# Kernel optimization log

Measured on AMD Instinct MI355X. Metric: run time of the kernel, lower is better.

Reference implementation:

```python
import jax, jax.numpy as jnp
import numpy as np

TEMP = 0.5      # init temperature
EPS = 1e-8      # torch CosineSimilarity eps
B = 4096
D = 512


def setup_inputs() -> dict:
    key = jax.random.key(0)
    k1, k2 = jax.random.split(key)
    return {
        "zis": jax.random.normal(k1, (B, D), dtype=jnp.float32),
        "zjs": jax.random.normal(k2, (B, D), dtype=jnp.float32),
    }


def reference(zis, zjs):
    # representations = cat([zjs, zis]) -> [2B, D]
    reps = jnp.concatenate([zjs, zis], axis=0)
    b = zis.shape[0]
    n = 2 * b

    # cosine similarity matrix [2B, 2B]
    norms = jnp.maximum(jnp.linalg.norm(reps, axis=-1, keepdims=True), EPS)
    z = reps / norms
    sim = jnp.matmul(z, z.T) / TEMP

    # positive for row i is sim[i, (i+B) % 2B]; self-similarity is excluded.
    # CE with label 0 over [pos, negatives] == logsumexp over row (minus diag)
    # minus the positive logit, because pos is exactly the masked pair entry.
    idx = jnp.arange(n)
    pair = (idx + b) % n
    pos = sim[idx, pair]
    sim_masked = jnp.where(jnp.eye(n, dtype=bool), -1e9, sim)  # drop diagonal
    per_row = jax.nn.logsumexp(sim_masked, axis=-1) - pos
    # criterion sums, then divides by 2B -> mean
    return jnp.mean(per_row)
```

## Files before the change

kernel.cpp:

```cpp
#include <hip/hip_runtime.h>

#define N_TOT 8192
#define BHALF 4096
#define D_DIM 512
#define BM 128
#define BK 64
#define NTILE 64
#define NBLOCKS 2080

typedef float f32x4 __attribute__((ext_vector_type(4)));
typedef short s16x8 __attribute__((ext_vector_type(8)));

__device__ __forceinline__ unsigned short f2bf(float x) {
    union { float f; unsigned int u; } v; v.f = x;
    unsigned int lsb = (v.u >> 16) & 1u;
    unsigned int r = v.u + 0x7fffu + lsb;
    return (unsigned short)(r >> 16);
}

__global__ __launch_bounds__(256) void normalize_kernel(
    const float* __restrict__ zis, const float* __restrict__ zjs,
    unsigned short* __restrict__ zb, float* __restrict__ rowsum)
{
    if (blockIdx.x < 32) rowsum[blockIdx.x * 256 + threadIdx.x] = 0.0f;
    int wave = threadIdx.x >> 6;
    int lane = threadIdx.x & 63;
    int row  = blockIdx.x * 4 + wave;
    const float* src = (row < BHALF) ? (zjs + (size_t)row * D_DIM)
                                     : (zis + (size_t)(row - BHALF) * D_DIM);
    const float4* src4 = (const float4*)src;
    float4 v0 = src4[lane * 2];
    float4 v1 = src4[lane * 2 + 1];
    float ss = v0.x*v0.x + v0.y*v0.y + v0.z*v0.z + v0.w*v0.w
             + v1.x*v1.x + v1.y*v1.y + v1.z*v1.z + v1.w*v1.w;
    #pragma unroll
    for (int off = 1; off < 64; off <<= 1) ss += __shfl_xor(ss, off);
    float scale = 1.0f / fmaxf(sqrtf(ss), 1e-8f);

    float vals[8] = {v0.x, v0.y, v0.z, v0.w, v1.x, v1.y, v1.z, v1.w};
    unsigned short u[8];
    #pragma unroll
    for (int i = 0; i < 8; ++i) u[i] = f2bf(vals[i] * scale);
    uint4 o;
    o.x = u[0] | ((unsigned)u[1] << 16);
    o.y = u[2] | ((unsigned)u[3] << 16);
    o.z = u[4] | ((unsigned)u[5] << 16);
    o.w = u[6] | ((unsigned)u[7] << 16);
    ((uint4*)(zb + (size_t)row * D_DIM))[lane] = o;
}

__global__ __launch_bounds__(256) void ntxent_tri_kernel(
    const unsigned short* __restrict__ zb, float* __restrict__ rowsum,
    float* __restrict__ pos_ws)
{
    __shared__ unsigned short As[BM * BK];
    __shared__ unsigned short Bs[BM * BK];
    __shared__ float rsum_lds[BM];
    __shared__ float csum_lds[BM];

    const int tid  = threadIdx.x;
    const int wave = tid >> 6;
    const int lane = tid & 63;
    const int cq   = lane & 15;
    const int quad = lane >> 4;
    const int wr   = wave >> 1;
    const int wc   = wave & 1;

    int g = 0, rem = blockIdx.x;
    while (rem >= 64 * g + 36) { rem -= 64 * g + 36; ++g; }
    int I, J;
    if (rem < 64 * g) { I = rem >> 3; J = 8 * g + (rem & 7); }
    else {
        rem -= 64 * g;
        int ii = 0;
        while (rem >= 8 - ii) { rem -= 8 - ii; ++ii; }
        I = 8 * g + ii;
        J = I + rem;
    }
    const int rowbase = I * BM;
    const int colbase = J * BM;
    const bool diagblk = (I == J);
    const bool posblk  = (J == I + NTILE / 2);

    if (tid < BM) { rsum_lds[tid] = 0.0f; csum_lds[tid] = 0.0f; }

    const int r0  = tid >> 3;
    const int c8s = (tid & 7) ^ (r0 & 7);
    const unsigned short* gA[4];
    const unsigned short* gB[4];
    #pragma unroll
    for (int rnd = 0; rnd < 4; ++rnd) {
        int r = rnd * 32 + r0;
        gA[rnd] = zb + (size_t)(rowbase + r) * D_DIM + c8s * 8;
        gB[rnd] = zb + (size_t)(colbase + r) * D_DIM + c8s * 8;
    }

    int aOff[4], aSw[4], bOff[4], bSw[4];
    #pragma unroll
    for (int t = 0; t < 4; ++t) {
        int ra = wr * 64 + t * 16 + cq;
        int rb = wc * 64 + t * 16 + cq;
        aOff[t] = ra * 64; aSw[t] = ra & 7;
        bOff[t] = rb * 64; bSw[t] = rb & 7;
    }

    f32x4 acc[4][4];
    #pragma unroll
    for (int a = 0; a < 4; ++a)
        #pragma unroll
        for (int b = 0; b < 4; ++b)
            acc[a][b] = (f32x4){0.f, 0.f, 0.f, 0.f};

    for (int kc = 0; kc < D_DIM / BK; ++kc) {
        __syncthreads();
        #pragma unroll
        for (int rnd = 0; rnd < 4; ++rnd) {
            __builtin_amdgcn_global_load_lds(
                (const __attribute__((address_space(1))) unsigned int*)gA[rnd],
                (__attribute__((address_space(3))) unsigned int*)&As[(rnd * 256 + tid) * 8],
                16, 0, 0);
            __builtin_amdgcn_global_load_lds(
                (const __attribute__((address_space(1))) unsigned int*)gB[rnd],
                (__attribute__((address_space(3))) unsigned int*)&Bs[(rnd * 256 + tid) * 8],
                16, 0, 0);
            gA[rnd] += BK; gB[rnd] += BK;
        }
        __syncthreads();

        #pragma unroll
        for (int kk = 0; kk < 2; ++kk) {
            s16x8 af[4], bf[4];
            const int c8a = kk * 4 + quad;
            #pragma unroll
            for (int t = 0; t < 4; ++t) {
                af[t] = *(const s16x8*)&As[aOff[t] + ((c8a ^ aSw[t]) << 3)];
                bf[t] = *(const s16x8*)&Bs[bOff[t] + ((c8a ^ bSw[t]) << 3)];
            }
            #pragma unroll
            for (int ar = 0; ar < 4; ++ar)
                #pragma unroll
                for (int bc = 0; bc < 4; ++bc)
                    acc[ar][bc] = __builtin_amdgcn_mfma_f32_16x16x32_bf16(
                        af[ar], bf[bc], acc[ar][bc], 0, 0, 0);
        }
    }

    if (posblk && wc == wr) {
        #pragma unroll
        for (int ar = 0; ar < 4; ++ar)
            #pragma unroll
            for (int reg = 0; reg < 4; ++reg)
                if (cq == quad * 4 + reg) {
                    int gr = rowbase + wr * 64 + ar * 16 + quad * 4 + reg;
                    pos_ws[gr] = acc[ar][ar][reg] * 2.0f;
                }
    }

    #pragma unroll
    for (int ar = 0; ar < 4; ++ar)
        #pragma unroll
        for (int bc = 0; bc < 4; ++bc)
            #pragma unroll
            for (int reg = 0; reg < 4; ++reg)
                acc[ar][bc][reg] = __expf(acc[ar][bc][reg] * 2.0f);
    if (diagblk && wr == wc) {
        #pragma unroll
        for (int ar = 0; ar < 4; ++ar)
            #pragma unroll
            for (int reg = 0; reg < 4; ++reg)
                if (cq == quad * 4 + reg) acc[ar][ar][reg] = 0.0f;
    }

    #pragma unroll
    for (int ar = 0; ar < 4; ++ar) {
        float rs[4];
        #pragma unroll
        for (int reg = 0; reg < 4; ++reg) {
            float v = acc[ar][0][reg] + acc[ar][1][reg] + acc[ar][2][reg] + acc[ar][3][reg];
            v += __shfl_xor(v, 1); v += __shfl_xor(v, 2);
            v += __shfl_xor(v, 4); v += __shfl_xor(v, 8);
            rs[reg] = v;
        }
        if (cq == 0) {
            #pragma unroll
            for (int reg = 0; reg < 4; ++reg)
                atomicAdd(&rsum_lds[wr * 64 + ar * 16 + quad * 4 + reg], rs[reg]);
        }
    }

    if (!diagblk) {
        #pragma unroll
        for (int bc = 0; bc < 4; ++bc) {
            float cs = 0.0f;
            #pragma unroll
            for (int ar = 0; ar < 4; ++ar)
                #pragma unroll
                for (int reg = 0; reg < 4; ++reg)
                    cs += acc[ar][bc][reg];
            cs += __shfl_xor(cs, 16); cs += __shfl_xor(cs, 32);
            if (quad == 0) atomicAdd(&csum_lds[wc * 64 + bc * 16 + cq], cs);
        }
    }

    __syncthreads();
    if (tid < BM) atomicAdd(&rowsum[rowbase + tid], rsum_lds[tid]);
    else if (!diagblk) atomicAdd(&rowsum[colbase + tid - BM], csum_lds[tid - BM]);
}

__global__ __launch_bounds__(256) void finalize_kernel(
    const float* __restrict__ rowsum, const float* __restrict__ pos_ws,
    float* __restrict__ out)
{
    __shared__ float red[4];
    float s = 0.0f;
    for (int r = threadIdx.x; r < N_TOT; r += 256)
        s += __logf(rowsum[r]) - pos_ws[r & (BHALF - 1)];
    #pragma unroll
    for (int off = 1; off < 64; off <<= 1) s += __shfl_xor(s, off);
    int wave = threadIdx.x >> 6, lane = threadIdx.x & 63;
    if (lane == 0) red[wave] = s;
    __syncthreads();
    if (threadIdx.x == 0)
        out[0] = (red[0] + red[1] + red[2] + red[3]) * (1.0f / N_TOT);
}

extern "C" void kernel_launch(void* const* d_in, const int* in_sizes, int n_in,
                              void* d_out, int out_size, void* d_ws, size_t ws_size,
                              hipStream_t stream) {
    const float* zis = (const float*)d_in[0];
    const float* zjs = (const float*)d_in[1];
    float* rowsum = (float*)d_ws;
    float* pos_ws = (float*)d_ws + N_TOT;
    unsigned short* zb = (unsigned short*)((float*)d_ws + N_TOT + BHALF);
    float* out = (float*)d_out;

    normalize_kernel<<<N_TOT / 4, 256, 0, stream>>>(zis, zjs, zb, rowsum);
    ntxent_tri_kernel<<<NBLOCKS, 256, 0, stream>>>(zb, rowsum, pos_ws);
    finalize_kernel<<<1, 256, 0, stream>>>(rowsum, pos_ws, out);
}
```

Measured before the change: 132.3 us.

## Fuse finalize into GEMM via last-block counter, fold scale into exp2

Folds the 1/T and log2(e) factors into the normalization scale (sqrt(2/ln2)) so the epilogue can use a raw exp2 instead of multiply plus expf, and rescales the positive logit by ln2. The finalize kernel is removed: a done counter lets the last block finishing the triangular GEMM compute the log-sum reduction, saving one launch. LDS for the row and column sums now reuses the A tile buffer, and launch bounds request 5 waves per SIMD. This adds extra barriers, a global atomic counter and fences, and the pre-scaled bf16 inputs change rounding slightly.

New measurement: 182.1 us. 1.38x slower.

```diff
diff --git a/kernel.cpp b/kernel.cpp
--- a/kernel.cpp
+++ b/kernel.cpp
@@ -8,6 +8,9 @@
 #define NTILE 64
 #define NBLOCKS 2080
 
+#define ZSCALE 1.69864368f
+#define LN2F   0.69314718f
+
 typedef float f32x4 __attribute__((ext_vector_type(4)));
 typedef short s16x8 __attribute__((ext_vector_type(8)));
 
@@ -18,11 +21,21 @@
     return (unsigned short)(r >> 16);
 }
 
+__device__ __forceinline__ float fast_exp2(float x) {
+#if __has_builtin(__builtin_amdgcn_exp2f)
+    return __builtin_amdgcn_exp2f(x);
+#else
+    return exp2f(x);
+#endif
+}
+
 __global__ __launch_bounds__(256) void normalize_kernel(
     const float* __restrict__ zis, const float* __restrict__ zjs,
-    unsigned short* __restrict__ zb, float* __restrict__ rowsum)
+    unsigned short* __restrict__ zb, float* __restrict__ rowsum,
+    unsigned int* __restrict__ done_ctr)
 {
     if (blockIdx.x < 32) rowsum[blockIdx.x * 256 + threadIdx.x] = 0.0f;
+    if (blockIdx.x == 32 && threadIdx.x == 0) *done_ctr = 0u;
     int wave = threadIdx.x >> 6;
     int lane = threadIdx.x & 63;
     int row  = blockIdx.x * 4 + wave;
@@ -35,7 +48,7 @@
              + v1.x*v1.x + v1.y*v1.y + v1.z*v1.z + v1.w*v1.w;
     #pragma unroll
     for (int off = 1; off < 64; off <<= 1) ss += __shfl_xor(ss, off);
-    float scale = 1.0f / fmaxf(sqrtf(ss), 1e-8f);
+    float scale = ZSCALE / fmaxf(sqrtf(ss), 1e-8f);
 
     float vals[8] = {v0.x, v0.y, v0.z, v0.w, v1.x, v1.y, v1.z, v1.w};
     unsigned short u[8];
@@ -49,14 +62,13 @@
     ((uint4*)(zb + (size_t)row * D_DIM))[lane] = o;
 }
 
-__global__ __launch_bounds__(256) void ntxent_tri_kernel(
+__global__ __launch_bounds__(256, 5) void ntxent_tri_kernel(
     const unsigned short* __restrict__ zb, float* __restrict__ rowsum,
-    float* __restrict__ pos_ws)
+    float* __restrict__ pos_ws, float* __restrict__ out,
+    unsigned int* __restrict__ done_ctr)
 {
     __shared__ unsigned short As[BM * BK];
     __shared__ unsigned short Bs[BM * BK];
-    __shared__ float rsum_lds[BM];
-    __shared__ float csum_lds[BM];
 
     const int tid  = threadIdx.x;
     const int wave = tid >> 6;
@@ -82,8 +94,6 @@
     const bool diagblk = (I == J);
     const bool posblk  = (J == I + NTILE / 2);
 
-    if (tid < BM) { rsum_lds[tid] = 0.0f; csum_lds[tid] = 0.0f; }
-
     const int r0  = tid >> 3;
     const int c8s = (tid & 7) ^ (r0 & 7);
     const unsigned short* gA[4];
@@ -152,7 +162,8 @@
             for (int reg = 0; reg < 4; ++reg)
                 if (cq == quad * 4 + reg) {
                     int gr = rowbase + wr * 64 + ar * 16 + quad * 4 + reg;
-                    pos_ws[gr] = acc[ar][ar][reg] * 2.0f;
+                    __hip_atomic_store(&pos_ws[gr], acc[ar][ar][reg] * LN2F,
+                                       __ATOMIC_RELAXED, __HIP_MEMORY_SCOPE_AGENT);
                 }
     }
 
@@ -162,7 +173,7 @@
         for (int bc = 0; bc < 4; ++bc)
             #pragma unroll
             for (int reg = 0; reg < 4; ++reg)
-                acc[ar][bc][reg] = __expf(acc[ar][bc][reg] * 2.0f);
+                acc[ar][bc][reg] = fast_exp2(acc[ar][bc][reg]);
     if (diagblk && wr == wc) {
         #pragma unroll
         for (int ar = 0; ar < 4; ++ar)
@@ -170,6 +181,12 @@
             for (int reg = 0; reg < 4; ++reg)
                 if (cq == quad * 4 + reg) acc[ar][ar][reg] = 0.0f;
     }
+
+    float* rsum_lds = (float*)As;
+    float* csum_lds = rsum_lds + BM;
+    __syncthreads();
+    ((float*)As)[tid] = 0.0f;
+    __syncthreads();
 
     #pragma unroll
     for (int ar = 0; ar < 4; ++ar) {
@@ -205,23 +222,32 @@
     __syncthreads();
     if (tid < BM) atomicAdd(&rowsum[rowbase + tid], rsum_lds[tid]);
     else if (!diagblk) atomicAdd(&rowsum[colbase + tid - BM], csum_lds[tid - BM]);
-}
-
-__global__ __launch_bounds__(256) void finalize_kernel(
-    const float* __restrict__ rowsum, const float* __restrict__ pos_ws,
-    float* __restrict__ out)
-{
-    __shared__ float red[4];
-    float s = 0.0f;
-    for (int r = threadIdx.x; r < N_TOT; r += 256)
-        s += __logf(rowsum[r]) - pos_ws[r & (BHALF - 1)];
-    #pragma unroll
-    for (int off = 1; off < 64; off <<= 1) s += __shfl_xor(s, off);
-    int wave = threadIdx.x >> 6, lane = threadIdx.x & 63;
-    if (lane == 0) red[wave] = s;
-    __syncthreads();
-    if (threadIdx.x == 0)
-        out[0] = (red[0] + red[1] + red[2] + red[3]) * (1.0f / N_TOT);
+
+    __shared__ int lastflag;
+    __syncthreads();
+    if (tid == 0) {
+        __threadfence();
+        lastflag = (atomicAdd(done_ctr, 1u) == (unsigned)(NBLOCKS - 1));
+    }
+    __syncthreads();
+    if (lastflag) {
+        __threadfence();
+        float s = 0.0f;
+        for (int r = tid; r < N_TOT; r += 256) {
+            float rsv = __hip_atomic_load(&rowsum[r],
+                                          __ATOMIC_RELAXED, __HIP_MEMORY_SCOPE_AGENT);
+            float pv  = __hip_atomic_load(&pos_ws[r & (BHALF - 1)],
+                                          __ATOMIC_RELAXED, __HIP_MEMORY_SCOPE_AGENT);
+            s += __logf(rsv) - pv;
+        }
+        #pragma unroll
+        for (int off = 1; off < 64; off <<= 1) s += __shfl_xor(s, off);
+        float* red = (float*)Bs;
+        if ((tid & 63) == 0) red[tid >> 6] = s;
+        __syncthreads();
+        if (tid == 0)
+            out[0] = (red[0] + red[1] + red[2] + red[3]) * (1.0f / N_TOT);
+    }
 }
 
 extern "C" void kernel_launch(void* const* d_in, const int* in_sizes, int n_in,
@@ -230,11 +256,11 @@
     const float* zis = (const float*)d_in[0];
     const float* zjs = (const float*)d_in[1];
     float* rowsum = (float*)d_ws;
-    float* pos_ws = (float*)d_ws + N_TOT;
-    unsigned short* zb = (unsigned short*)((float*)d_ws + N_TOT + BHALF);
+    float* pos_ws = rowsum + N_TOT;
+    unsigned int* done_ctr = (unsigned int*)(pos_ws + BHALF);
+    unsigned short* zb = (unsigned short*)(pos_ws + BHALF + 4);
     float* out = (float*)d_out;
 
-    normalize_kernel<<<N_TOT / 4, 256, 0, stream>>>(zis, zjs, zb, rowsum);
-    ntxent_tri_kernel<<<NBLOCKS, 256, 0, stream>>>(zb, rowsum, pos_ws);
-    finalize_kernel<<<1, 256, 0, stream>>>(rowsum, pos_ws, out);
-}
+    normalize_kernel<<<N_TOT / 4, 256, 0, stream>>>(zis, zjs, zb, rowsum, done_ctr);
+    ntxent_tri_kernel<<<NBLOCKS, 256, 0, stream>>>(zb, rowsum, pos_ws, out, done_ctr);
+}
```

## Double-buffer K loop with smaller chunks and fold temperature into normalization for exp2

Applied to the files above, without the earlier changes.

The GEMM main loop now uses two LDS buffers of 32-wide K chunks and issues the next chunk's global-to-LDS loads before computing the current one, gated by a partial vmcnt wait. This is meant to overlap memory latency with MFMA work instead of fully synchronising every chunk. The normalized vectors are pre-scaled by sqrt(2/ln2), so the dot product is already in log2 units and the epilogue uses a raw exp2 instead of a multiply plus exp. The positive logit is rescaled by ln2. The reduction scratch now reuses the A buffer to save LDS. Scaling before bf16 rounding slightly changes numerics.

After: 123.7 us. -6.5%, faster.

```diff
diff --git a/kernel.cpp b/kernel.cpp
--- a/kernel.cpp
+++ b/kernel.cpp
@@ -4,9 +4,14 @@
 #define BHALF 4096
 #define D_DIM 512
 #define BM 128
-#define BK 64
 #define NTILE 64
 #define NBLOCKS 2080
+#define BK2 32
+#define NCHUNK 16
+#define BUFSZ (BM * BK2)
+
+#define ZSCALE 1.69864368f
+#define LN2F   0.69314718f
 
 typedef float f32x4 __attribute__((ext_vector_type(4)));
 typedef short s16x8 __attribute__((ext_vector_type(8)));
@@ -16,6 +21,14 @@
     unsigned int lsb = (v.u >> 16) & 1u;
     unsigned int r = v.u + 0x7fffu + lsb;
     return (unsigned short)(r >> 16);
+}
+
+__device__ __forceinline__ float fast_exp2(float x) {
+#if __has_builtin(__builtin_amdgcn_exp2f)
+    return __builtin_amdgcn_exp2f(x);
+#else
+    return exp2f(x);
+#endif
 }
 
 __global__ __launch_bounds__(256) void normalize_kernel(
@@ -35,7 +48,7 @@
              + v1.x*v1.x + v1.y*v1.y + v1.z*v1.z + v1.w*v1.w;
     #pragma unroll
     for (int off = 1; off < 64; off <<= 1) ss += __shfl_xor(ss, off);
-    float scale = 1.0f / fmaxf(sqrtf(ss), 1e-8f);
+    float scale = ZSCALE / fmaxf(sqrtf(ss), 1e-8f);
 
     float vals[8] = {v0.x, v0.y, v0.z, v0.w, v1.x, v1.y, v1.z, v1.w};
     unsigned short u[8];
@@ -53,10 +66,8 @@
     const unsigned short* __restrict__ zb, float* __restrict__ rowsum,
     float* __restrict__ pos_ws)
 {
-    __shared__ unsigned short As[BM * BK];
-    __shared__ unsigned short Bs[BM * BK];
-    __shared__ float rsum_lds[BM];
-    __shared__ float csum_lds[BM];
+    __shared__ unsigned short As[2 * BUFSZ];
+    __shared__ unsigned short Bs[2 * BUFSZ];
 
     const int tid  = threadIdx.x;
     const int wave = tid >> 6;
@@ -82,26 +93,20 @@
     const bool diagblk = (I == J);
     const bool posblk  = (J == I + NTILE / 2);
 
-    if (tid < BM) { rsum_lds[tid] = 0.0f; csum_lds[tid] = 0.0f; }
-
-    const int r0  = tid >> 3;
-    const int c8s = (tid & 7) ^ (r0 & 7);
-    const unsigned short* gA[4];
-    const unsigned short* gB[4];
-    #pragma unroll
-    for (int rnd = 0; rnd < 4; ++rnd) {
-        int r = rnd * 32 + r0;
-        gA[rnd] = zb + (size_t)(rowbase + r) * D_DIM + c8s * 8;
-        gB[rnd] = zb + (size_t)(colbase + r) * D_DIM + c8s * 8;
-    }
-
-    int aOff[4], aSw[4], bOff[4], bSw[4];
+    const int c8s = (tid & 3) ^ ((tid >> 3) & 3);
+    const unsigned short* pA0 = zb + (size_t)(rowbase + (tid >> 2)) * D_DIM + c8s * 8;
+    const unsigned short* pA1 = pA0 + (size_t)64 * D_DIM;
+    const unsigned short* pB0 = zb + (size_t)(colbase + (tid >> 2)) * D_DIM + c8s * 8;
+    const unsigned short* pB1 = pB0 + (size_t)64 * D_DIM;
+    const int dst0 = tid * 8;
+    const int dst1 = (256 + tid) * 8;
+
+    const int swz = (quad ^ ((cq >> 1) & 3)) << 3;
+    int aOff[4], bOff[4];
     #pragma unroll
     for (int t = 0; t < 4; ++t) {
-        int ra = wr * 64 + t * 16 + cq;
-        int rb = wc * 64 + t * 16 + cq;
-        aOff[t] = ra * 64; aSw[t] = ra & 7;
-        bOff[t] = rb * 64; bSw[t] = rb & 7;
+        aOff[t] = (wr * 64 + t * 16 + cq) * BK2 + swz;
+        bOff[t] = (wc * 64 + t * 16 + cq) * BK2 + swz;
     }
 
     f32x4 acc[4][4];
@@ -111,39 +116,57 @@
         for (int b = 0; b < 4; ++b)
             acc[a][b] = (f32x4){0.f, 0.f, 0.f, 0.f};
 
-    for (int kc = 0; kc < D_DIM / BK; ++kc) {
-        __syncthreads();
-        #pragma unroll
-        for (int rnd = 0; rnd < 4; ++rnd) {
-            __builtin_amdgcn_global_load_lds(
-                (const __attribute__((address_space(1))) unsigned int*)gA[rnd],
-                (__attribute__((address_space(3))) unsigned int*)&As[(rnd * 256 + tid) * 8],
-                16, 0, 0);
-            __builtin_amdgcn_global_load_lds(
-                (const __attribute__((address_space(1))) unsigned int*)gB[rnd],
-                (__attribute__((address_space(3))) unsigned int*)&Bs[(rnd * 256 + tid) * 8],
-                16, 0, 0);
-            gA[rnd] += BK; gB[rnd] += BK;
-        }
-        __syncthreads();
-
-        #pragma unroll
-        for (int kk = 0; kk < 2; ++kk) {
-            s16x8 af[4], bf[4];
-            const int c8a = kk * 4 + quad;
-            #pragma unroll
-            for (int t = 0; t < 4; ++t) {
-                af[t] = *(const s16x8*)&As[aOff[t] + ((c8a ^ aSw[t]) << 3)];
-                bf[t] = *(const s16x8*)&Bs[bOff[t] + ((c8a ^ bSw[t]) << 3)];
-            }
-            #pragma unroll
-            for (int ar = 0; ar < 4; ++ar)
-                #pragma unroll
-                for (int bc = 0; bc < 4; ++bc)
-                    acc[ar][bc] = __builtin_amdgcn_mfma_f32_16x16x32_bf16(
-                        af[ar], bf[bc], acc[ar][bc], 0, 0, 0);
-        }
-    }
+#define STAGE(buf) do {                                                          \
+    const int dbase = (buf) * BUFSZ;                                             \
+    __builtin_amdgcn_global_load_lds(                                            \
+        (const __attribute__((address_space(1))) unsigned int*)pA0,              \
+        (__attribute__((address_space(3))) unsigned int*)&As[dbase + dst0],      \
+        16, 0, 0);                                                               \
+    __builtin_amdgcn_global_load_lds(                                            \
+        (const __attribute__((address_space(1))) unsigned int*)pA1,              \
+        (__attribute__((address_space(3))) unsigned int*)&As[dbase + dst1],      \
+        16, 0, 0);                                                               \
+    __builtin_amdgcn_global_load_lds(                                            \
+        (const __attribute__((address_space(1))) unsigned int*)pB0,              \
+        (__attribute__((address_space(3))) unsigned int*)&Bs[dbase + dst0],      \
+        16, 0, 0);                                                               \
+    __builtin_amdgcn_global_load_lds(                                            \
+        (const __attribute__((address_space(1))) unsigned int*)pB1,              \
+        (__attribute__((address_space(3))) unsigned int*)&Bs[dbase + dst1],      \
+        16, 0, 0);                                                               \
+    pA0 += BK2; pA1 += BK2; pB0 += BK2; pB1 += BK2;                              \
+} while (0)
+
+#define COMPUTE(buf) do {                                                        \
+    const int cbase = (buf) * BUFSZ;                                             \
+    s16x8 af[4], bf[4];                                                          \
+    _Pragma("unroll")                                                            \
+    for (int t = 0; t < 4; ++t) {                                                \
+        af[t] = *(const s16x8*)&As[cbase + aOff[t]];                             \
+        bf[t] = *(const s16x8*)&Bs[cbase + bOff[t]];                             \
+    }                                                                            \
+    _Pragma("unroll")                                                            \
+    for (int ar = 0; ar < 4; ++ar)                                               \
+        _Pragma("unroll")                                                        \
+        for (int bc = 0; bc < 4; ++bc)                                           \
+            acc[ar][bc] = __builtin_amdgcn_mfma_f32_16x16x32_bf16(               \
+                af[ar], bf[bc], acc[ar][bc], 0, 0, 0);                           \
+} while (0)
+
+    STAGE(0);
+    #pragma unroll
+    for (int kc = 0; kc < NCHUNK - 1; ++kc) {
+        STAGE((kc + 1) & 1);
+        asm volatile("s_waitcnt vmcnt(4)" ::: "memory");
+        __builtin_amdgcn_s_barrier();
+        __builtin_amdgcn_sched_barrier(0);
+        COMPUTE(kc & 1);
+        __builtin_amdgcn_s_barrier();
+    }
+    asm volatile("s_waitcnt vmcnt(0)" ::: "memory");
+    __builtin_amdgcn_s_barrier();
+    __builtin_amdgcn_sched_barrier(0);
+    COMPUTE((NCHUNK - 1) & 1);
 
     if (posblk && wc == wr) {
         #pragma unroll
@@ -152,7 +175,7 @@
             for (int reg = 0; reg < 4; ++reg)
                 if (cq == quad * 4 + reg) {
                     int gr = rowbase + wr * 64 + ar * 16 + quad * 4 + reg;
-                    pos_ws[gr] = acc[ar][ar][reg] * 2.0f;
+                    pos_ws[gr] = acc[ar][ar][reg] * LN2F;
                 }
     }
 
@@ -162,7 +185,7 @@
         for (int bc = 0; bc < 4; ++bc)
             #pragma unroll
             for (int reg = 0; reg < 4; ++reg)
-                acc[ar][bc][reg] = __expf(acc[ar][bc][reg] * 2.0f);
+                acc[ar][bc][reg] = fast_exp2(acc[ar][bc][reg]);
     if (diagblk && wr == wc) {
         #pragma unroll
         for (int ar = 0; ar < 4; ++ar)
@@ -170,6 +193,12 @@
             for (int reg = 0; reg < 4; ++reg)
                 if (cq == quad * 4 + reg) acc[ar][ar][reg] = 0.0f;
     }
+
+    float* rsum_lds = (float*)As;
+    float* csum_lds = rsum_lds + BM;
+    __syncthreads();
+    ((float*)As)[tid] = 0.0f;
+    __syncthreads();
 
     #pragma unroll
     for (int ar = 0; ar < 4; ++ar) {
@@ -205,6 +234,8 @@
     __syncthreads();
     if (tid < BM) atomicAdd(&rowsum[rowbase + tid], rsum_lds[tid]);
     else if (!diagblk) atomicAdd(&rowsum[colbase + tid - BM], csum_lds[tid - BM]);
+#undef STAGE
+#undef COMPUTE
 }
 
 __global__ __launch_bounds__(256) void finalize_kernel(
@@ -230,8 +261,8 @@
     const float* zis = (const float*)d_in[0];
     const float* zjs = (const float*)d_in[1];
     float* rowsum = (float*)d_ws;
-    float* pos_ws = (float*)d_ws + N_TOT;
-    unsigned short* zb = (unsigned short*)((float*)d_ws + N_TOT + BHALF);
+    float* pos_ws = rowsum + N_TOT;
+    unsigned short* zb = (unsigned short*)(pos_ws + BHALF);
     float* out = (float*)d_out;
 
     normalize_kernel<<<N_TOT / 4, 256, 0, stream>>>(zis, zjs, zb, rowsum);
```

## Drop LDS staging, load MFMA fragments from global, and fold temperature into exp2

Applied to the files above, without the earlier changes.

The similarity kernel no longer stages A/B tiles through shared memory with global_load_lds and barriers. Each lane now reads its bf16 MFMA fragments straight from global memory, relying on L1/L2 for reuse, and the K loop is fully unrolled. Block indices are remapped to group neighbouring tiles for L2 locality, and the normalization pre-scales vectors by sqrt(2/ln2) so the epilogue can use a bare exp2 with no multiply; the positive logit is rescaled by ln2 to match. The risk is redundant, less coalesced global traffic, since waves sharing a row tile each fetch it, plus slightly different bf16 rounding from the pre-scale.

Measured after the change: 208.7 us. +57.8%, slower.

```diff
diff --git a/kernel.cpp b/kernel.cpp
--- a/kernel.cpp
+++ b/kernel.cpp
@@ -4,9 +4,13 @@
 #define BHALF 4096
 #define D_DIM 512
 #define BM 128
-#define BK 64
 #define NTILE 64
 #define NBLOCKS 2080
+#define BK2 32
+#define NCHUNK 16
+
+#define ZSCALE 1.69864368f
+#define LN2F   0.69314718f
 
 typedef float f32x4 __attribute__((ext_vector_type(4)));
 typedef short s16x8 __attribute__((ext_vector_type(8)));
@@ -16,6 +20,14 @@
     unsigned int lsb = (v.u >> 16) & 1u;
     unsigned int r = v.u + 0x7fffu + lsb;
     return (unsigned short)(r >> 16);
+}
+
+__device__ __forceinline__ float fast_exp2(float x) {
+#if __has_builtin(__builtin_amdgcn_exp2f)
+    return __builtin_amdgcn_exp2f(x);
+#else
+    return exp2f(x);
+#endif
 }
 
 __global__ __launch_bounds__(256) void normalize_kernel(
@@ -35,7 +47,7 @@
              + v1.x*v1.x + v1.y*v1.y + v1.z*v1.z + v1.w*v1.w;
     #pragma unroll
     for (int off = 1; off < 64; off <<= 1) ss += __shfl_xor(ss, off);
-    float scale = 1.0f / fmaxf(sqrtf(ss), 1e-8f);
+    float scale = ZSCALE / fmaxf(sqrtf(ss), 1e-8f);
 
     float vals[8] = {v0.x, v0.y, v0.z, v0.w, v1.x, v1.y, v1.z, v1.w};
     unsigned short u[8];
@@ -53,10 +65,7 @@
     const unsigned short* __restrict__ zb, float* __restrict__ rowsum,
     float* __restrict__ pos_ws)
 {
-    __shared__ unsigned short As[BM * BK];
-    __shared__ unsigned short Bs[BM * BK];
-    __shared__ float rsum_lds[BM];
-    __shared__ float csum_lds[BM];
+    __shared__ float sum_lds[256];
 
     const int tid  = threadIdx.x;
     const int wave = tid >> 6;
@@ -66,7 +75,12 @@
     const int wr   = wave >> 1;
     const int wc   = wave & 1;
 
-    int g = 0, rem = blockIdx.x;
+    sum_lds[tid] = 0.0f;
+    __syncthreads();
+
+    const int swzbid = (blockIdx.x & 7) * (NBLOCKS / 8) + (blockIdx.x >> 3);
+
+    int g = 0, rem = swzbid;
     while (rem >= 64 * g + 36) { rem -= 64 * g + 36; ++g; }
     int I, J;
     if (rem < 64 * g) { I = rem >> 3; J = 8 * g + (rem & 7); }
@@ -82,26 +96,12 @@
     const bool diagblk = (I == J);
     const bool posblk  = (J == I + NTILE / 2);
 
-    if (tid < BM) { rsum_lds[tid] = 0.0f; csum_lds[tid] = 0.0f; }
-
-    const int r0  = tid >> 3;
-    const int c8s = (tid & 7) ^ (r0 & 7);
-    const unsigned short* gA[4];
-    const unsigned short* gB[4];
-    #pragma unroll
-    for (int rnd = 0; rnd < 4; ++rnd) {
-        int r = rnd * 32 + r0;
-        gA[rnd] = zb + (size_t)(rowbase + r) * D_DIM + c8s * 8;
-        gB[rnd] = zb + (size_t)(colbase + r) * D_DIM + c8s * 8;
-    }
-
-    int aOff[4], aSw[4], bOff[4], bSw[4];
+    const unsigned short* pA[4];
+    const unsigned short* pB[4];
     #pragma unroll
     for (int t = 0; t < 4; ++t) {
-        int ra = wr * 64 + t * 16 + cq;
-        int rb = wc * 64 + t * 16 + cq;
-        aOff[t] = ra * 64; aSw[t] = ra & 7;
-        bOff[t] = rb * 64; bSw[t] = rb & 7;
+        pA[t] = zb + (size_t)(rowbase + wr * 64 + t * 16 + cq) * D_DIM + quad * 8;
+        pB[t] = zb + (size_t)(colbase + wc * 64 + t * 16 + cq) * D_DIM + quad * 8;
     }
 
     f32x4 acc[4][4];
@@ -111,38 +111,20 @@
         for (int b = 0; b < 4; ++b)
             acc[a][b] = (f32x4){0.f, 0.f, 0.f, 0.f};
 
-    for (int kc = 0; kc < D_DIM / BK; ++kc) {
-        __syncthreads();
-        #pragma unroll
-        for (int rnd = 0; rnd < 4; ++rnd) {
-            __builtin_amdgcn_global_load_lds(
-                (const __attribute__((address_space(1))) unsigned int*)gA[rnd],
-                (__attribute__((address_space(3))) unsigned int*)&As[(rnd * 256 + tid) * 8],
-                16, 0, 0);
-            __builtin_amdgcn_global_load_lds(
-                (const __attribute__((address_space(1))) unsigned int*)gB[rnd],
-                (__attribute__((address_space(3))) unsigned int*)&Bs[(rnd * 256 + tid) * 8],
-                16, 0, 0);
-            gA[rnd] += BK; gB[rnd] += BK;
-        }
-        __syncthreads();
-
-        #pragma unroll
-        for (int kk = 0; kk < 2; ++kk) {
-            s16x8 af[4], bf[4];
-            const int c8a = kk * 4 + quad;
-            #pragma unroll
-            for (int t = 0; t < 4; ++t) {
-                af[t] = *(const s16x8*)&As[aOff[t] + ((c8a ^ aSw[t]) << 3)];
-                bf[t] = *(const s16x8*)&Bs[bOff[t] + ((c8a ^ bSw[t]) << 3)];
-            }
-            #pragma unroll
-            for (int ar = 0; ar < 4; ++ar)
-                #pragma unroll
-                for (int bc = 0; bc < 4; ++bc)
-                    acc[ar][bc] = __builtin_amdgcn_mfma_f32_16x16x32_bf16(
-                        af[ar], bf[bc], acc[ar][bc], 0, 0, 0);
-        }
+    #pragma unroll
+    for (int kc = 0; kc < NCHUNK; ++kc) {
+        s16x8 af[4], bf[4];
+        #pragma unroll
+        for (int t = 0; t < 4; ++t) {
+            af[t] = *(const s16x8*)(pA[t] + kc * BK2);
+            bf[t] = *(const s16x8*)(pB[t] + kc * BK2);
+        }
+        #pragma unroll
+        for (int ar = 0; ar < 4; ++ar)
+            #pragma unroll
+            for (int bc = 0; bc < 4; ++bc)
+                acc[ar][bc] = __builtin_amdgcn_mfma_f32_16x16x32_bf16(
+                    af[ar], bf[bc], acc[ar][bc], 0, 0, 0);
     }
 
     if (posblk && wc == wr) {
@@ -152,7 +134,7 @@
             for (int reg = 0; reg < 4; ++reg)
                 if (cq == quad * 4 + reg) {
                     int gr = rowbase + wr * 64 + ar * 16 + quad * 4 + reg;
-                    pos_ws[gr] = acc[ar][ar][reg] * 2.0f;
+                    pos_ws[gr] = acc[ar][ar][reg] * LN2F;
                 }
     }
 
@@ -162,7 +144,7 @@
         for (int bc = 0; bc < 4; ++bc)
             #pragma unroll
             for (int reg = 0; reg < 4; ++reg)
-                acc[ar][bc][reg] = __expf(acc[ar][bc][reg] * 2.0f);
+                acc[ar][bc][reg] = fast_exp2(acc[ar][bc][reg]);
     if (diagblk && wr == wc) {
         #pragma unroll
         for (int ar = 0; ar < 4; ++ar)
@@ -170,6 +152,9 @@
             for (int reg = 0; reg < 4; ++reg)
                 if (cq == quad * 4 + reg) acc[ar][ar][reg] = 0.0f;
     }
+
+    float* rsum_lds = sum_lds;
+    float* csum_lds = sum_lds + BM;
 
     #pragma unroll
     for (int ar = 0; ar < 4; ++ar) {
@@ -230,8 +215,8 @@
     const float* zis = (const float*)d_in[0];
     const float* zjs = (const float*)d_in[1];
     float* rowsum = (float*)d_ws;
-    float* pos_ws = (float*)d_ws + N_TOT;
-    unsigned short* zb = (unsigned short*)((float*)d_ws + N_TOT + BHALF);
+    float* pos_ws = rowsum + N_TOT;
+    unsigned short* zb = (unsigned short*)(pos_ws + BHALF);
     float* out = (float*)d_out;
 
     normalize_kernel<<<N_TOT / 4, 256, 0, stream>>>(zis, zjs, zb, rowsum);
```
